# Performance work log

Measured on AMD Instinct MI355X. Metric: run time of the kernel, lower is better.

The kernel has to match this reference:

```python
import jax, jax.numpy as jnp
import numpy as np

V, DM, DEPTH, N = 50257, 512, 8, 16  # vocab, dim, depth, ssm_dim
B, L = 2, 1024
GATE = 0.5  # fixed_gate=True blend


def layer_norm(x, g, b):
    mu = x.mean(-1, keepdims=True)
    xm = x - mu
    var = (xm * xm).mean(-1, keepdims=True)
    return xm * jax.lax.rsqrt(var + 1e-5) * g + b


def ssm(u, W_dt, b_dt, W_B, W_C, A_log, D_p):
    # selective SSM: h_t = exp(dt_t*A)*h_{t-1} + dt_t*B_t*u_t ; y_t = C_t.h_t + D*u_t
    dt = jax.nn.softplus(u @ W_dt + b_dt)            # (B,L,DM)
    Bm = u @ W_B                                      # (B,L,N)
    Cm = u @ W_C                                      # (B,L,N)
    A = -jnp.exp(A_log)                               # (DM,N), stable (negative)

    def step(h, inp):
        dt_t, B_t, C_t, u_t = inp                     # (B,DM),(B,N),(B,N),(B,DM)
        h = jnp.exp(dt_t[..., None] * A) * h + (dt_t * u_t)[..., None] * B_t[:, None, :]
        y = jnp.einsum('bdn,bn->bd', h, C_t)
        return h, y

    h0 = jnp.zeros((u.shape[0], DM, N), u.dtype)
    xs = (dt.transpose(1, 0, 2), Bm.transpose(1, 0, 2), Cm.transpose(1, 0, 2), u.transpose(1, 0, 2))
    _, ys = jax.lax.scan(step, h0, xs)
    return ys.transpose(1, 0, 2) + D_p * u


def wkv(x, W_r, W_k, W_v, W_o, t_decay, t_first):
    # RWKV-4 channel-wise WKV recurrence
    r = jax.nn.sigmoid(x @ W_r)
    k = jnp.clip(x @ W_k, -30.0, 30.0)
    v = x @ W_v
    w = jnp.exp(-jnp.exp(t_decay))                    # (DM,) decay in (0,1)

    def step(carry, inp):
        a, b = carry
        k_t, v_t = inp
        ek = jnp.exp(k_t)
        eu = jnp.exp(t_first + k_t)
        out = (a + eu * v_t) / (b + eu + 1e-6)
        return (w * a + ek * v_t, w * b + ek), out

    a0 = jnp.zeros((x.shape[0], DM), x.dtype)
    _, o = jax.lax.scan(step, (a0, jnp.zeros_like(a0)), (k.transpose(1, 0, 2), v.transpose(1, 0, 2)))
    return (r * o.transpose(1, 0, 2)) @ W_o


def setup_inputs() -> dict:
    key = jax.random.key(0)
    ks = jax.random.split(key, 16)
    s = 0.02
    inp = {
        'input_ids': jax.random.randint(ks[0], (B, L), 0, V, dtype=jnp.int32),
        'emb': jax.random.normal(ks[1], (V, DM), jnp.float32) * s,
        'ln1_g': jnp.ones((DEPTH, DM), jnp.float32),
        'ln1_b': jnp.zeros((DEPTH, DM), jnp.float32),
        'W_dt': jax.random.normal(ks[2], (DEPTH, DM, DM), jnp.float32) * s,
        'b_dt': jnp.zeros((DEPTH, DM), jnp.float32),
        'W_B': jax.random.normal(ks[3], (DEPTH, DM, N), jnp.float32) * s,
        'W_C': jax.random.normal(ks[4], (DEPTH, DM, N), jnp.float32) * s,
        'A_log': jnp.broadcast_to(jnp.log(jnp.arange(1, N + 1, dtype=jnp.float32)), (DEPTH, DM, N)).copy(),
        'D_p': jnp.ones((DEPTH, DM), jnp.float32),
        'ln2_g': jnp.ones((DEPTH, DM), jnp.float32),
        'ln2_b': jnp.zeros((DEPTH, DM), jnp.float32),
        'W_r': jax.random.normal(ks[5], (DEPTH, DM, DM), jnp.float32) * s,
        'W_k': jax.random.normal(ks[6], (DEPTH, DM, DM), jnp.float32) * s,
        'W_v': jax.random.normal(ks[7], (DEPTH, DM, DM), jnp.float32) * s,
        'W_o': jax.random.normal(ks[8], (DEPTH, DM, DM), jnp.float32) * s,
        't_decay': jax.random.normal(ks[9], (DEPTH, DM), jnp.float32) * 0.5,
        't_first': jax.random.normal(ks[10], (DEPTH, DM), jnp.float32) * 0.5,
        'lnf_g': jnp.ones((DM,), jnp.float32),
        'lnf_b': jnp.zeros((DM,), jnp.float32),
    }
    return inp


def reference(input_ids, emb, ln1_g, ln1_b, W_dt, b_dt, W_B, W_C, A_log, D_p,
              ln2_g, ln2_b, W_r, W_k, W_v, W_o, t_decay, t_first, lnf_g, lnf_b):
    x = emb[input_ids]                                # (B,L,DM)
    for i in range(DEPTH):
        x = x + GATE * ssm(layer_norm(x, ln1_g[i], ln1_b[i]),
                           W_dt[i], b_dt[i], W_B[i], W_C[i], A_log[i], D_p[i])
        x = x + GATE * wkv(layer_norm(x, ln2_g[i], ln2_b[i]),
                           W_r[i], W_k[i], W_v[i], W_o[i], t_decay[i], t_first[i])
    x = layer_norm(x, lnf_g, lnf_b)
    logits = x @ emb.T                                # tied LM head, (B,L,V)
    return logits
```

## Files before the change

kernel.cpp:

```cpp
#include <hip/hip_runtime.h>

#define DM 512
#define NST 16
#define NDEPTH 8
#define NB 2
#define NL 1024
#define MROWS 2048
#define VOCAB 50257
#define VPAD  50304
#define NCH 32
#define CLEN 32

typedef __attribute__((ext_vector_type(8))) short bf16x8;
typedef __attribute__((ext_vector_type(4))) float f32x4;
typedef __attribute__((ext_vector_type(8))) unsigned short ushort8;

#define AS1(p) ((const __attribute__((address_space(1))) void*)(p))
#define AS3(p) ((__attribute__((address_space(3))) void*)(p))

static __device__ __forceinline__ unsigned short f2bf(float f) {
  unsigned int x = __float_as_uint(f);
  unsigned int r = (x + 0x7FFFu + ((x >> 16) & 1u)) >> 16;
  return (unsigned short)r;
}

__global__ __launch_bounds__(256) void k_gather(const int* __restrict__ ids,
    const float* __restrict__ emb, float* __restrict__ x)
{
  int gid = blockIdx.x * 256 + threadIdx.x;
  int row = gid >> 7, c = (gid & 127) * 4;
  int id = ids[row];
  *(float4*)(x + (size_t)row * DM + c) = *(const float4*)(emb + (size_t)id * DM + c);
}

__global__ void k_transpose(const float* __restrict__ Wdt, const float* __restrict__ Wr,
    const float* __restrict__ Wk, const float* __restrict__ Wv, const float* __restrict__ Wo,
    unsigned short* __restrict__ Tdtbc, unsigned short* __restrict__ Trkv, unsigned short* __restrict__ To)
{
  __shared__ float tile[32][33];
  int z = blockIdx.z, layer = z / 5, f = z % 5;
  const float* src;
  unsigned short* dst;
  size_t lw = (size_t)layer * DM * DM;
  if (f == 0)      { src = Wdt + lw; dst = Tdtbc + (size_t)layer * 640 * DM; }
  else if (f == 1) { src = Wr  + lw; dst = Trkv + (size_t)layer * 3 * DM * DM; }
  else if (f == 2) { src = Wk  + lw; dst = Trkv + (size_t)layer * 3 * DM * DM + DM * DM; }
  else if (f == 3) { src = Wv  + lw; dst = Trkv + (size_t)layer * 3 * DM * DM + 2 * DM * DM; }
  else             { src = Wo  + lw; dst = To   + lw; }
  int tx = threadIdx.x, ty = threadIdx.y;
  int kb = blockIdx.y * 32, nb = blockIdx.x * 32;
  #pragma unroll
  for (int i = 0; i < 4; i++)
    tile[ty + i * 8][tx] = src[(size_t)(kb + ty + i * 8) * DM + nb + tx];
  __syncthreads();
  #pragma unroll
  for (int i = 0; i < 4; i++)
    dst[(size_t)(nb + ty + i * 8) * DM + kb + tx] = f2bf(tile[tx][ty + i * 8]);
}

__global__ __launch_bounds__(256) void k_bcpack(const float* __restrict__ WB,
    const float* __restrict__ WC, unsigned short* __restrict__ Tdtbc)
{
  int gid = blockIdx.x * 256 + threadIdx.x;
  int k = gid & 511, n = (gid >> 9) & 127, layer = gid >> 16;
  float v = 0.f;
  if (n < 16)      v = WB[((size_t)layer * DM + k) * NST + n];
  else if (n < 32) v = WC[((size_t)layer * DM + k) * NST + (n - 16)];
  Tdtbc[(size_t)layer * 640 * DM + (size_t)(512 + n) * DM + k] = f2bf(v);
}

__global__ __launch_bounds__(256) void k_embcvt(const float* __restrict__ emb,
    unsigned short* __restrict__ out)
{
  int gid = blockIdx.x * 256 + threadIdx.x;
  size_t base = (size_t)gid * 8;
  int row = (int)(base >> 9);
  ushort8 o;
  if (row < VOCAB) {
    float4 a = *(const float4*)(emb + base);
    float4 b = *(const float4*)(emb + base + 4);
    o[0]=f2bf(a.x); o[1]=f2bf(a.y); o[2]=f2bf(a.z); o[3]=f2bf(a.w);
    o[4]=f2bf(b.x); o[5]=f2bf(b.y); o[6]=f2bf(b.z); o[7]=f2bf(b.w);
  } else {
    o = (ushort8)0;
  }
  *(ushort8*)(out + base) = o;
}

__global__ __launch_bounds__(256) void k_ln(const float* __restrict__ x,
    const float* __restrict__ g, const float* __restrict__ bb,
    float* __restrict__ of, unsigned short* __restrict__ ob)
{
  const int w = threadIdx.x >> 6, l = threadIdx.x & 63;
  const int row = blockIdx.x * 4 + w;
  const float* xr = x + (size_t)row * DM + l * 8;
  float4 v0 = *(const float4*)(xr);
  float4 v1 = *(const float4*)(xr + 4);
  float s = v0.x + v0.y + v0.z + v0.w + v1.x + v1.y + v1.z + v1.w;
  float q = v0.x*v0.x + v0.y*v0.y + v0.z*v0.z + v0.w*v0.w
          + v1.x*v1.x + v1.y*v1.y + v1.z*v1.z + v1.w*v1.w;
  #pragma unroll
  for (int m = 1; m < 64; m <<= 1) { s += __shfl_xor(s, m); q += __shfl_xor(q, m); }
  const float mu = s * (1.0f / DM);
  const float var = q * (1.0f / DM) - mu * mu;
  const float rs = rsqrtf(var + 1e-5f);
  const float4 g0 = *(const float4*)(g + l * 8);
  const float4 g1 = *(const float4*)(g + l * 8 + 4);
  const float4 b0 = *(const float4*)(bb + l * 8);
  const float4 b1 = *(const float4*)(bb + l * 8 + 4);
  float y[8];
  y[0] = (v0.x - mu) * rs * g0.x + b0.x;
  y[1] = (v0.y - mu) * rs * g0.y + b0.y;
  y[2] = (v0.z - mu) * rs * g0.z + b0.z;
  y[3] = (v0.w - mu) * rs * g0.w + b0.w;
  y[4] = (v1.x - mu) * rs * g1.x + b1.x;
  y[5] = (v1.y - mu) * rs * g1.y + b1.y;
  y[6] = (v1.z - mu) * rs * g1.z + b1.z;
  y[7] = (v1.w - mu) * rs * g1.w + b1.w;
  if (of) {
    float4 o0 = {y[0], y[1], y[2], y[3]}, o1 = {y[4], y[5], y[6], y[7]};
    *(float4*)(of + (size_t)row * DM + l * 8) = o0;
    *(float4*)(of + (size_t)row * DM + l * 8 + 4) = o1;
  }
  if (ob) {
    ushort8 o;
    #pragma unroll
    for (int j = 0; j < 8; j++) o[j] = f2bf(y[j]);
    *(ushort8*)(ob + (size_t)row * DM + l * 8) = o;
  }
}

template<int BM, int BN, int EPI>
__global__ __launch_bounds__(256) void gemm_bt(const unsigned short* __restrict__ A,
    const unsigned short* __restrict__ Bt, float* __restrict__ C, int N, int ldc,
    const float* __restrict__ bias, float* __restrict__ C2)
{
  constexpr int K = DM;
  constexpr int MI = BM / 32, NI = BN / 32;
  __shared__ unsigned short lsA[BM * 64];
  __shared__ unsigned short lsB[BN * 64];
  const int t = threadIdx.x;
  const int w = t >> 6, l = t & 63;
  const int wm = (w >> 1) * (BM / 2), wn = (w & 1) * (BN / 2);
  const size_t bm = (size_t)blockIdx.x * BM, bn = (size_t)blockIdx.y * BN;
  f32x4 acc[MI][NI] = {};
  const int srow = t >> 3, sslot = t & 7;
  const int gs = sslot ^ (srow & 7);
  const unsigned short* Ag = A + (bm + srow) * K + gs * 8;
  const unsigned short* Bg = Bt + (bn + srow) * K + gs * 8;
  const int lr = l & 15, lq = l >> 4;
  for (int k0 = 0; k0 < K; k0 += 64) {
    #pragma unroll
    for (int o = 0; o < BM / 32; ++o)
      __builtin_amdgcn_global_load_lds(AS1(Ag + (size_t)(o * 32) * K + k0),
          AS3(lsA + (o * 32 + srow) * 64 + sslot * 8), 16, 0, 0);
    #pragma unroll
    for (int o = 0; o < BN / 32; ++o)
      __builtin_amdgcn_global_load_lds(AS1(Bg + (size_t)(o * 32) * K + k0),
          AS3(lsB + (o * 32 + srow) * 64 + sslot * 8), 16, 0, 0);
    asm volatile("s_waitcnt vmcnt(0)" ::: "memory");
    __syncthreads();
    bf16x8 af[MI][2], bfr[NI][2];
    #pragma unroll
    for (int i = 0; i < MI; ++i) {
      int row = wm + i * 16 + lr;
      #pragma unroll
      for (int h = 0; h < 2; ++h)
        af[i][h] = *(const bf16x8*)(lsA + row * 64 + (((h * 4 + lq) ^ (row & 7)) * 8));
    }
    #pragma unroll
    for (int i = 0; i < NI; ++i) {
      int row = wn + i * 16 + lr;
      #pragma unroll
      for (int h = 0; h < 2; ++h)
        bfr[i][h] = *(const bf16x8*)(lsB + row * 64 + (((h * 4 + lq) ^ (row & 7)) * 8));
    }
    #pragma unroll
    for (int h = 0; h < 2; ++h)
      #pragma unroll
      for (int mi = 0; mi < MI; ++mi)
        #pragma unroll
        for (int ni = 0; ni < NI; ++ni)
          acc[mi][ni] = __builtin_amdgcn_mfma_f32_16x16x32_bf16(af[mi][h], bfr[ni][h], acc[mi][ni], 0, 0, 0);
    __syncthreads();
  }
  const int lg = l >> 4;
  #pragma unroll
  for (int mi = 0; mi < MI; ++mi) {
    #pragma unroll
    for (int ni = 0; ni < NI; ++ni) {
      int n = (int)bn + wn + ni * 16 + lr;
      size_t m0 = bm + wm + mi * 16 + lg * 4;
      #pragma unroll
      for (int j = 0; j < 4; ++j) {
        float v = acc[mi][ni][j];
        if (EPI == 0) {
          C[(m0 + j) * (size_t)ldc + n] = v;
        } else if (EPI == 2) {
          C2[(m0 + j) * (size_t)ldc + n] += 0.5f * v;
        } else {
          if (n < 512) {
            float b = v + bias[n];
            C[(m0 + j) * (size_t)512 + n] = fmaxf(b, 0.f) + log1pf(__expf(-fabsf(b)));
          } else if (n < 544) {
            C2[(m0 + j) * (size_t)32 + (n - 512)] = v;
          }
        }
      }
    }
  }
}

__global__ __launch_bounds__(512) void gemm_head(const unsigned short* __restrict__ A,
    const unsigned short* __restrict__ Bt, float* __restrict__ C)
{
  __shared__ unsigned short lsA[256 * 64];
  __shared__ unsigned short lsB[128 * 64];
  const int t = threadIdx.x;
  const int w = t >> 6, l = t & 63;
  const int wm = (w >> 1) * 64, wn = (w & 1) * 64;
  const int c = (int)blockIdx.x & 7, j = (int)blockIdx.x >> 3;
  const int ntile = c * 50 + (j >> 3), mtile = j & 7;
  if (ntile >= 393) return;
  const size_t bm = (size_t)mtile * 256, bn = (size_t)ntile * 128;
  f32x4 acc[4][4] = {};
  const int srow = t >> 3, sslot = t & 7;
  const int gs = sslot ^ (srow & 7);
  const unsigned short* Ag = A + (bm + srow) * DM + gs * 8;
  const unsigned short* Bg = Bt + (bn + srow) * DM + gs * 8;
  const int lr = l & 15, lq = l >> 4;
  for (int k0 = 0; k0 < DM; k0 += 64) {
    #pragma unroll
    for (int o = 0; o < 4; ++o)
      __builtin_amdgcn_global_load_lds(AS1(Ag + (size_t)(o * 64) * DM + k0),
          AS3(lsA + (o * 64 + srow) * 64 + sslot * 8), 16, 0, 0);
    #pragma unroll
    for (int o = 0; o < 2; ++o)
      __builtin_amdgcn_global_load_lds(AS1(Bg + (size_t)(o * 64) * DM + k0),
          AS3(lsB + (o * 64 + srow) * 64 + sslot * 8), 16, 0, 0);
    asm volatile("s_waitcnt vmcnt(0)" ::: "memory");
    __syncthreads();
    bf16x8 af[4][2], bfr[4][2];
    #pragma unroll
    for (int i = 0; i < 4; ++i) {
      int row = wm + i * 16 + lr;
      #pragma unroll
      for (int h = 0; h < 2; ++h)
        af[i][h] = *(const bf16x8*)(lsA + row * 64 + (((h * 4 + lq) ^ (row & 7)) * 8));
    }
    #pragma unroll
    for (int i = 0; i < 4; ++i) {
      int row = wn + i * 16 + lr;
      #pragma unroll
      for (int h = 0; h < 2; ++h)
        bfr[i][h] = *(const bf16x8*)(lsB + row * 64 + (((h * 4 + lq) ^ (row & 7)) * 8));
    }
    #pragma unroll
    for (int h = 0; h < 2; ++h)
      #pragma unroll
      for (int mi = 0; mi < 4; ++mi)
        #pragma unroll
        for (int ni = 0; ni < 4; ++ni)
          acc[mi][ni] = __builtin_amdgcn_mfma_f32_16x16x32_bf16(af[mi][h], bfr[ni][h], acc[mi][ni], 0, 0, 0);
    __syncthreads();
  }
  const int lg = l >> 4;
  #pragma unroll
  for (int mi = 0; mi < 4; ++mi) {
    #pragma unroll
    for (int ni = 0; ni < 4; ++ni) {
      int n = (int)bn + wn + ni * 16 + lr;
      if (n >= VOCAB) continue;
      size_t m0 = bm + wm + mi * 16 + lg * 4;
      #pragma unroll
      for (int jj = 0; jj < 4; ++jj)
        C[(m0 + jj) * (size_t)VOCAB + n] = acc[mi][ni][jj];
    }
  }
}

__global__ __launch_bounds__(256) void k_ssm1(const float* __restrict__ dt,
    const float* __restrict__ u, const float* __restrict__ BC,
    const float* __restrict__ A_log, float* __restrict__ Pb, float* __restrict__ Sb)
{
  const int t = threadIdx.x;
  const int grp = t >> 4, n = t & 15;
  const int cg = blockIdx.x & 63, ck = blockIdx.x >> 6;
  const int ch = cg * 16 + grp;
  const int b = ch >> 9, d = ch & 511;
  const float A = -__expf(A_log[d * NST + n]);
  const int t0 = ck * CLEN;
  const float* dtp = dt + ((size_t)b * NL + t0) * DM + d;
  const float* up  = u  + ((size_t)b * NL + t0) * DM + d;
  const float* bcp = BC + ((size_t)b * NL + t0) * 32 + n;
  float P = 1.f, S = 0.f;
  #pragma unroll
  for (int tt = 0; tt < CLEN; ++tt) {
    float dtv = dtp[(size_t)tt * DM];
    float uv  = up[(size_t)tt * DM];
    float Bv  = bcp[(size_t)tt * 32];
    float e = __expf(dtv * A);
    S = fmaf(e, S, dtv * uv * Bv);
    P *= e;
  }
  size_t cn = (size_t)ch * NST + n;
  Pb[cn * NCH + ck] = P;
  Sb[cn * NCH + ck] = S;
}

__global__ __launch_bounds__(256) void k_ssm2(const float* __restrict__ Pb,
    const float* __restrict__ Sb, float* __restrict__ H0)
{
  const int wid = blockIdx.x * 8 + (threadIdx.x >> 5);
  const int lane = threadIdx.x & 31;
  float coef = Pb[(size_t)wid * NCH + lane];
  float sum  = Sb[(size_t)wid * NCH + lane];
  #pragma unroll
  for (int m = 1; m < 32; m <<= 1) {
    float cr = __shfl_up(coef, m, 32);
    float sr = __shfl_up(sum, m, 32);
    if (lane >= m) { sum = fmaf(coef, sr, sum); coef *= cr; }
  }
  float hp = __shfl_up(sum, 1, 32);
  H0[(size_t)wid * NCH + lane] = (lane == 0) ? 0.f : hp;
}

__global__ __launch_bounds__(256) void k_ssm3(const float* __restrict__ dt,
    const float* __restrict__ u, const float* __restrict__ BC,
    const float* __restrict__ A_log, const float* __restrict__ Dp,
    const float* __restrict__ H0, float* __restrict__ x)
{
  const int t = threadIdx.x;
  const int grp = t >> 4, n = t & 15;
  const int cg = blockIdx.x & 63, ck = blockIdx.x >> 6;
  const int ch = cg * 16 + grp;
  const int b = ch >> 9, d = ch & 511;
  const float A = -__expf(A_log[d * NST + n]);
  const float Dpv = Dp[d];
  const int t0 = ck * CLEN;
  const float* dtp = dt + ((size_t)b * NL + t0) * DM + d;
  const float* up  = u  + ((size_t)b * NL + t0) * DM + d;
  const float* bcp = BC + ((size_t)b * NL + t0) * 32 + n;
  float* xp = x + ((size_t)b * NL + t0) * DM + d;
  size_t cn = (size_t)ch * NST + n;
  float h = H0[cn * NCH + ck];
  #pragma unroll
  for (int tt = 0; tt < CLEN; ++tt) {
    float dtv = dtp[(size_t)tt * DM];
    float uv  = up[(size_t)tt * DM];
    float Bv  = bcp[(size_t)tt * 32];
    float Cv  = bcp[(size_t)tt * 32 + 16];
    float e = __expf(dtv * A);
    h = fmaf(e, h, dtv * uv * Bv);
    float p2 = h * Cv;
    p2 += __shfl_xor(p2, 1);
    p2 += __shfl_xor(p2, 2);
    p2 += __shfl_xor(p2, 4);
    p2 += __shfl_xor(p2, 8);
    if (n == 0) xp[(size_t)tt * DM] += 0.5f * (p2 + Dpv * uv);
  }
}

__global__ __launch_bounds__(256) void k_wkv1(const float* __restrict__ rkv,
    const float* __restrict__ tdec, float* __restrict__ SaB, float* __restrict__ SbB)
{
  const int gid = blockIdx.x * 256 + threadIdx.x;
  const int ch = gid & 1023, ck = gid >> 10;
  const int b = ch >> 9, d = ch & 511;
  const float w = __expf(-__expf(tdec[d]));
  const float* base = rkv + ((size_t)b * NL + ck * CLEN) * 1536;
  float Sa = 0.f, Sb = 0.f;
  #pragma unroll
  for (int tt = 0; tt < CLEN; ++tt) {
    const float* row = base + (size_t)tt * 1536;
    float kt = row[512 + d];
    kt = fminf(30.f, fmaxf(-30.f, kt));
    float vt = row[1024 + d];
    float ek = __expf(kt);
    Sa = fmaf(w, Sa, ek * vt);
    Sb = fmaf(w, Sb, ek);
  }
  SaB[(size_t)ch * NCH + ck] = Sa;
  SbB[(size_t)ch * NCH + ck] = Sb;
}

__global__ __launch_bounds__(256) void k_wkv2(const float* __restrict__ SaB,
    const float* __restrict__ SbB, const float* __restrict__ tdec,
    float* __restrict__ HaB, float* __restrict__ HbB)
{
  const int ch = blockIdx.x * 8 + (threadIdx.x >> 5);
  const int lane = threadIdx.x & 31;
  const int d = ch & 511;
  float coef = __expf(-32.f * __expf(tdec[d]));
  float sa = SaB[(size_t)ch * NCH + lane];
  float sb = SbB[(size_t)ch * NCH + lane];
  #pragma unroll
  for (int m = 1; m < 32; m <<= 1) {
    float cr  = __shfl_up(coef, m, 32);
    float sar = __shfl_up(sa, m, 32);
    float sbr = __shfl_up(sb, m, 32);
    if (lane >= m) { sa = fmaf(coef, sar, sa); sb = fmaf(coef, sbr, sb); coef *= cr; }
  }
  float ha = __shfl_up(sa, 1, 32);
  float hb = __shfl_up(sb, 1, 32);
  HaB[(size_t)ch * NCH + lane] = (lane == 0) ? 0.f : ha;
  HbB[(size_t)ch * NCH + lane] = (lane == 0) ? 0.f : hb;
}

__global__ __launch_bounds__(256) void k_wkv3(const float* __restrict__ rkv,
    const float* __restrict__ tdec, const float* __restrict__ tfir,
    const float* __restrict__ HaB, const float* __restrict__ HbB,
    unsigned short* __restrict__ ro)
{
  const int gid = blockIdx.x * 256 + threadIdx.x;
  const int ch = gid & 1023, ck = gid >> 10;
  const int b = ch >> 9, d = ch & 511;
  const float w = __expf(-__expf(tdec[d]));
  const float tf = tfir[d];
  float a = HaB[(size_t)ch * NCH + ck];
  float bden = HbB[(size_t)ch * NCH + ck];
  const int t0 = ck * CLEN;
  const float* base = rkv + ((size_t)b * NL + t0) * 1536;
  unsigned short* rop = ro + ((size_t)b * NL + t0) * DM + d;
  #pragma unroll
  for (int tt = 0; tt < CLEN; ++tt) {
    const float* row = base + (size_t)tt * 1536;
    float rv = row[d];
    float kt = row[512 + d];
    kt = fminf(30.f, fmaxf(-30.f, kt));
    float vt = row[1024 + d];
    float ek = __expf(kt);
    float eu = __expf(tf + kt);
    float out = __fdividef(a + eu * vt, bden + eu + 1e-6f);
    float sig = __fdividef(1.f, 1.f + __expf(-rv));
    rop[(size_t)tt * DM] = f2bf(sig * out);
    a = fmaf(w, a, ek * vt);
    bden = fmaf(w, bden, ek);
  }
}

extern "C" void kernel_launch(void* const* d_in, const int* in_sizes, int n_in,
                              void* d_out, int out_size, void* d_ws, size_t ws_size,
                              hipStream_t stream)
{
  const int*   ids   = (const int*)d_in[0];
  const float* emb   = (const float*)d_in[1];
  const float* ln1_g = (const float*)d_in[2];
  const float* ln1_b = (const float*)d_in[3];
  const float* W_dt  = (const float*)d_in[4];
  const float* b_dt  = (const float*)d_in[5];
  const float* W_B   = (const float*)d_in[6];
  const float* W_C   = (const float*)d_in[7];
  const float* A_log = (const float*)d_in[8];
  const float* D_p   = (const float*)d_in[9];
  const float* ln2_g = (const float*)d_in[10];
  const float* ln2_b = (const float*)d_in[11];
  const float* W_r   = (const float*)d_in[12];
  const float* W_k   = (const float*)d_in[13];
  const float* W_v   = (const float*)d_in[14];
  const float* W_o   = (const float*)d_in[15];
  const float* t_dec = (const float*)d_in[16];
  const float* t_fir = (const float*)d_in[17];
  const float* lnf_g = (const float*)d_in[18];
  const float* lnf_b = (const float*)d_in[19];

  char* p = (char*)d_ws;
  float*          xres  = (float*)(p + 0);
  float*          u32   = (float*)(p + 4194304);
  float*          dtb   = (float*)(p + 8388608);
  float*          rkv   = (float*)(p + 12582912);
  float*          BCb   = (float*)(p + 25165824);
  unsigned short* abuf  = (unsigned short*)(p + 25427968);
  unsigned short* Tdtbc = (unsigned short*)(p + 27525120);
  unsigned short* To    = (unsigned short*)(p + 32768000);
  unsigned short* Trkv  = (unsigned short*)(p + 36962304);
  unsigned short* Tem   = (unsigned short*)(p + 49545216);

  float* Pb  = rkv;
  float* Sb  = rkv + 524288;
  float* H0  = rkv + 1048576;
  float* SaB = dtb;
  float* SbB = dtb + 32768;
  float* HaB = dtb + 65536;
  float* HbB = dtb + 98304;

  k_gather<<<1024, 256, 0, stream>>>(ids, emb, xres);
  k_transpose<<<dim3(16, 16, 40), dim3(32, 8), 0, stream>>>(W_dt, W_r, W_k, W_v, W_o, Tdtbc, Trkv, To);
  k_bcpack<<<2048, 256, 0, stream>>>(W_B, W_C, Tdtbc);
  k_embcvt<<<12576, 256, 0, stream>>>(emb, Tem);

  for (int i = 0; i < NDEPTH; ++i) {
    k_ln<<<512, 256, 0, stream>>>(xres, ln1_g + i * DM, ln1_b + i * DM, u32, abuf);
    gemm_bt<64, 128, 3><<<dim3(32, 5), 256, 0, stream>>>(abuf,
        Tdtbc + (size_t)i * 640 * DM, dtb, 640, 512, b_dt + i * DM, BCb);
    k_ssm1<<<2048, 256, 0, stream>>>(dtb, u32, BCb, A_log + (size_t)i * DM * NST, Pb, Sb);
    k_ssm2<<<2048, 256, 0, stream>>>(Pb, Sb, H0);
    k_ssm3<<<2048, 256, 0, stream>>>(dtb, u32, BCb, A_log + (size_t)i * DM * NST,
        D_p + i * DM, H0, xres);
    k_ln<<<512, 256, 0, stream>>>(xres, ln2_g + i * DM, ln2_b + i * DM, nullptr, abuf);
    gemm_bt<64, 128, 0><<<dim3(32, 12), 256, 0, stream>>>(abuf,
        Trkv + (size_t)i * 3 * DM * DM, rkv, 1536, 1536, nullptr, nullptr);
    k_wkv1<<<128, 256, 0, stream>>>(rkv, t_dec + i * DM, SaB, SbB);
    k_wkv2<<<128, 256, 0, stream>>>(SaB, SbB, t_dec + i * DM, HaB, HbB);
    k_wkv3<<<128, 256, 0, stream>>>(rkv, t_dec + i * DM, t_fir + i * DM, HaB, HbB, abuf);
    gemm_bt<64, 128, 2><<<dim3(32, 4), 256, 0, stream>>>(abuf,
        To + (size_t)i * DM * DM, nullptr, 512, 512, nullptr, xres);
  }

  k_ln<<<512, 256, 0, stream>>>(xres, lnf_g, lnf_b, nullptr, abuf);
  gemm_head<<<3200, 512, 0, stream>>>(abuf, Tem, (float*)d_out);
}
```

Measured before the change: 1.120 ms.

## Fuse chunk-prefix scan into SSM and WKV apply kernels, stage SSM output in LDS

Removes the separate parallel-scan kernels for the SSM and WKV chunked recurrences. Each apply-kernel thread now serially folds the preceding chunk summaries (up to 31 steps) to get its starting state, which saves two launches per layer and the intermediate state buffers. The SSM apply kernel also stages per-timestep outputs in shared memory and writes the residual update with more contiguous accesses. The cost is redundant serial prefix work in every thread, so later chunks take longer.

```diff
diff --git a/kernel.cpp b/kernel.cpp
--- a/kernel.cpp
+++ b/kernel.cpp
@@ -308,28 +308,13 @@
   Sb[cn * NCH + ck] = S;
 }
 
-__global__ __launch_bounds__(256) void k_ssm2(const float* __restrict__ Pb,
-    const float* __restrict__ Sb, float* __restrict__ H0)
-{
-  const int wid = blockIdx.x * 8 + (threadIdx.x >> 5);
-  const int lane = threadIdx.x & 31;
-  float coef = Pb[(size_t)wid * NCH + lane];
-  float sum  = Sb[(size_t)wid * NCH + lane];
-  #pragma unroll
-  for (int m = 1; m < 32; m <<= 1) {
-    float cr = __shfl_up(coef, m, 32);
-    float sr = __shfl_up(sum, m, 32);
-    if (lane >= m) { sum = fmaf(coef, sr, sum); coef *= cr; }
-  }
-  float hp = __shfl_up(sum, 1, 32);
-  H0[(size_t)wid * NCH + lane] = (lane == 0) ? 0.f : hp;
-}
-
-__global__ __launch_bounds__(256) void k_ssm3(const float* __restrict__ dt,
+__global__ __launch_bounds__(256) void k_ssm23(const float* __restrict__ dt,
     const float* __restrict__ u, const float* __restrict__ BC,
     const float* __restrict__ A_log, const float* __restrict__ Dp,
-    const float* __restrict__ H0, float* __restrict__ x)
-{
+    const float* __restrict__ Pb, const float* __restrict__ Sb,
+    float* __restrict__ x)
+{
+  __shared__ float ylds[CLEN][16];
   const int t = threadIdx.x;
   const int grp = t >> 4, n = t & 15;
   const int cg = blockIdx.x & 63, ck = blockIdx.x >> 6;
@@ -341,9 +326,11 @@
   const float* dtp = dt + ((size_t)b * NL + t0) * DM + d;
   const float* up  = u  + ((size_t)b * NL + t0) * DM + d;
   const float* bcp = BC + ((size_t)b * NL + t0) * 32 + n;
-  float* xp = x + ((size_t)b * NL + t0) * DM + d;
   size_t cn = (size_t)ch * NST + n;
-  float h = H0[cn * NCH + ck];
+  const float* Pp = Pb + cn * NCH;
+  const float* Sp = Sb + cn * NCH;
+  float h = 0.f;
+  for (int j = 0; j < ck; ++j) h = fmaf(Pp[j], h, Sp[j]);
   #pragma unroll
   for (int tt = 0; tt < CLEN; ++tt) {
     float dtv = dtp[(size_t)tt * DM];
@@ -357,7 +344,15 @@
     p2 += __shfl_xor(p2, 2);
     p2 += __shfl_xor(p2, 4);
     p2 += __shfl_xor(p2, 8);
-    if (n == 0) xp[(size_t)tt * DM] += 0.5f * (p2 + Dpv * uv);
+    if (n == 0) ylds[tt][grp] = 0.5f * (p2 + Dpv * uv);
+  }
+  __syncthreads();
+  const int d0 = (cg & 31) * 16;
+  float* xp = x + ((size_t)b * NL + t0) * DM + d0;
+  #pragma unroll
+  for (int idx = t; idx < CLEN * 16; idx += 256) {
+    int tt = idx >> 4, dd = idx & 15;
+    xp[(size_t)tt * DM + dd] += ylds[tt][dd];
   }
 }
 
@@ -384,32 +379,9 @@
   SbB[(size_t)ch * NCH + ck] = Sb;
 }
 
-__global__ __launch_bounds__(256) void k_wkv2(const float* __restrict__ SaB,
-    const float* __restrict__ SbB, const float* __restrict__ tdec,
-    float* __restrict__ HaB, float* __restrict__ HbB)
-{
-  const int ch = blockIdx.x * 8 + (threadIdx.x >> 5);
-  const int lane = threadIdx.x & 31;
-  const int d = ch & 511;
-  float coef = __expf(-32.f * __expf(tdec[d]));
-  float sa = SaB[(size_t)ch * NCH + lane];
-  float sb = SbB[(size_t)ch * NCH + lane];
-  #pragma unroll
-  for (int m = 1; m < 32; m <<= 1) {
-    float cr  = __shfl_up(coef, m, 32);
-    float sar = __shfl_up(sa, m, 32);
-    float sbr = __shfl_up(sb, m, 32);
-    if (lane >= m) { sa = fmaf(coef, sar, sa); sb = fmaf(coef, sbr, sb); coef *= cr; }
-  }
-  float ha = __shfl_up(sa, 1, 32);
-  float hb = __shfl_up(sb, 1, 32);
-  HaB[(size_t)ch * NCH + lane] = (lane == 0) ? 0.f : ha;
-  HbB[(size_t)ch * NCH + lane] = (lane == 0) ? 0.f : hb;
-}
-
-__global__ __launch_bounds__(256) void k_wkv3(const float* __restrict__ rkv,
+__global__ __launch_bounds__(256) void k_wkv23(const float* __restrict__ rkv,
     const float* __restrict__ tdec, const float* __restrict__ tfir,
-    const float* __restrict__ HaB, const float* __restrict__ HbB,
+    const float* __restrict__ SaB, const float* __restrict__ SbB,
     unsigned short* __restrict__ ro)
 {
   const int gid = blockIdx.x * 256 + threadIdx.x;
@@ -417,8 +389,14 @@
   const int b = ch >> 9, d = ch & 511;
   const float w = __expf(-__expf(tdec[d]));
   const float tf = tfir[d];
-  float a = HaB[(size_t)ch * NCH + ck];
-  float bden = HbB[(size_t)ch * NCH + ck];
+  const float W = __expf(-32.f * __expf(tdec[d]));
+  const float* Sap = SaB + (size_t)ch * NCH;
+  const float* Sbp = SbB + (size_t)ch * NCH;
+  float a = 0.f, bden = 0.f;
+  for (int j = 0; j < ck; ++j) {
+    a = fmaf(W, a, Sap[j]);
+    bden = fmaf(W, bden, Sbp[j]);
+  }
   const int t0 = ck * CLEN;
   const float* base = rkv + ((size_t)b * NL + t0) * 1536;
   unsigned short* rop = ro + ((size_t)b * NL + t0) * DM + d;
@@ -478,11 +456,8 @@
 
   float* Pb  = rkv;
   float* Sb  = rkv + 524288;
-  float* H0  = rkv + 1048576;
   float* SaB = dtb;
   float* SbB = dtb + 32768;
-  float* HaB = dtb + 65536;
-  float* HbB = dtb + 98304;
 
   k_gather<<<1024, 256, 0, stream>>>(ids, emb, xres);
   k_transpose<<<dim3(16, 16, 40), dim3(32, 8), 0, stream>>>(W_dt, W_r, W_k, W_v, W_o, Tdtbc, Trkv, To);
@@ -494,15 +469,13 @@
     gemm_bt<64, 128, 3><<<dim3(32, 5), 256, 0, stream>>>(abuf,
         Tdtbc + (size_t)i * 640 * DM, dtb, 640, 512, b_dt + i * DM, BCb);
     k_ssm1<<<2048, 256, 0, stream>>>(dtb, u32, BCb, A_log + (size_t)i * DM * NST, Pb, Sb);
-    k_ssm2<<<2048, 256, 0, stream>>>(Pb, Sb, H0);
-    k_ssm3<<<2048, 256, 0, stream>>>(dtb, u32, BCb, A_log + (size_t)i * DM * NST,
-        D_p + i * DM, H0, xres);
+    k_ssm23<<<2048, 256, 0, stream>>>(dtb, u32, BCb, A_log + (size_t)i * DM * NST,
+        D_p + i * DM, Pb, Sb, xres);
     k_ln<<<512, 256, 0, stream>>>(xres, ln2_g + i * DM, ln2_b + i * DM, nullptr, abuf);
     gemm_bt<64, 128, 0><<<dim3(32, 12), 256, 0, stream>>>(abuf,
         Trkv + (size_t)i * 3 * DM * DM, rkv, 1536, 1536, nullptr, nullptr);
     k_wkv1<<<128, 256, 0, stream>>>(rkv, t_dec + i * DM, SaB, SbB);
-    k_wkv2<<<128, 256, 0, stream>>>(SaB, SbB, t_dec + i * DM, HaB, HbB);
-    k_wkv3<<<128, 256, 0, stream>>>(rkv, t_dec + i * DM, t_fir + i * DM, HaB, HbB, abuf);
+    k_wkv23<<<128, 256, 0, stream>>>(rkv, t_dec + i * DM, t_fir + i * DM, SaB, SbB, abuf);
     gemm_bt<64, 128, 2><<<dim3(32, 4), 256, 0, stream>>>(abuf,
         To + (size_t)i * DM * DM, nullptr, 512, 512, nullptr, xres);
   }
```

New measurement: 1.452 ms. 29.7% more time.
